# Kernel tuning notes

Hardware: AMD Instinct MI355X
Metric: run time of the kernel (lower is better)

The kernel has to match this reference:

```python
import jax, jax.numpy as jnp
import numpy as np

NUM_HEADS = 4
NUM_LEVELS = 4
NUM_POINTS = 8
EMBED = 256
HEAD_DIM = EMBED // NUM_HEADS
SHAPES = np.array([[92, 160], [46, 80], [23, 40], [12, 20]], dtype=np.int64)  # (h, w) per level
NUM_VALUE = int((SHAPES[:, 0] * SHAPES[:, 1]).sum())  # 19560
DEPTH = 64
NQ = 20000
BS = 1
NZ = 4  # num_Z_anchors; NUM_POINTS % NZ == 0


def _depth_bias():
    # replicates init_smpl_off_weights for sampling_offsets_depth.bias
    th = np.arange(NUM_HEADS) * (2.0 * np.pi / NUM_HEADS)
    g = ((np.cos(th) + np.sin(th)) / 2.0)[:, None, None] * np.ones((NUM_HEADS, NUM_LEVELS, NUM_POINTS))
    g = g * (np.arange(NUM_POINTS) + 1)[None, None, :]
    return jnp.asarray(g.reshape(-1), dtype=jnp.float32)


def setup_inputs() -> dict:
    key = jax.random.key(0)
    ks = jax.random.split(key, 8)
    f = jnp.float32
    s = 0.02
    query = jax.random.normal(ks[0], (BS, NQ, EMBED), f)
    value = jax.random.normal(ks[1], (BS, NUM_VALUE, EMBED), f)
    value_dpt_dist = jax.nn.softmax(jax.random.normal(ks[2], (BS, NUM_VALUE, DEPTH), f), axis=-1)
    reference_points = jax.random.uniform(ks[3], (BS, NQ, NZ, 3), f)
    spatial_shapes = jnp.asarray(SHAPES)
    level_start_index = jnp.asarray(np.concatenate([[0], np.cumsum(SHAPES[:, 0] * SHAPES[:, 1])[:-1]]))
    Wv = jax.random.normal(ks[4], (EMBED, EMBED), f) * s
    bv = jnp.zeros((EMBED,), f)
    Wo = jax.random.normal(ks[5], (EMBED, NUM_HEADS * NUM_LEVELS * NUM_POINTS * 2), f) * s
    bo = jax.random.normal(ks[6], (NUM_HEADS * NUM_LEVELS * NUM_POINTS * 2,), f) * 0.5
    Wod = jnp.zeros((EMBED, NUM_HEADS * NUM_LEVELS * NUM_POINTS), f)  # constant_init 0.0
    bod = _depth_bias()
    Wa = jax.random.normal(ks[7], (EMBED, NUM_HEADS * NUM_LEVELS * NUM_POINTS), f) * s
    ba = jnp.zeros((NUM_HEADS * NUM_LEVELS * NUM_POINTS,), f)
    return dict(query=query, value=value, value_dpt_dist=value_dpt_dist,
                reference_points=reference_points, spatial_shapes=spatial_shapes,
                level_start_index=level_start_index, Wv=Wv, bv=bv, Wo=Wo, bo=bo,
                Wod=Wod, bod=bod, Wa=Wa, ba=ba)


def _forward(query, value, value_dpt_dist, reference_points, spatial_shapes,
             level_start_index, Wv, bv, Wo, bo, Wod, bod, Wa, ba):
    bs, nq, _ = query.shape
    H, L, P = NUM_HEADS, NUM_LEVELS, NUM_POINTS
    dh = HEAD_DIM
    D = value_dpt_dist.shape[-1]
    dt = query.dtype
    shapes = np.asarray(spatial_shapes)  # static level shapes

    v = (value @ Wv + bv).reshape(bs, -1, H, dh)  # value_proj
    off_uv = (query @ Wo + bo).reshape(bs, nq, H, L, P, 2)
    off_d = (query @ Wod + bod).reshape(bs, nq, H, L, P, 1)
    off = jnp.concatenate([off_uv, off_d], axis=-1)  # (bs,nq,H,L,P,3)
    attn = jax.nn.softmax((query @ Wa + ba).reshape(bs, nq, H, L * P), axis=-1)
    attn = attn.reshape(bs, nq, H, L, P)

    # offset_normalizer = (w, h, D) per level
    norm = jnp.asarray(np.stack([shapes[:, 1], shapes[:, 0], np.full(L, D)], -1), dtype=dt)
    off = off / norm[None, None, None, :, None, :]
    Z = reference_points.shape[2]
    off = off.reshape(bs, nq, H, L, P // Z, Z, 3)
    loc = (reference_points[:, :, None, None, None, :, :] + off).reshape(bs, nq, H, L, P, 3)

    starts = np.concatenate([[0], np.cumsum(shapes[:, 0] * shapes[:, 1])]).astype(int)
    gather_bh = jax.vmap(jax.vmap(lambda a, i: a[i]))   # over (bs, heads)
    gather_b = jax.vmap(lambda a, i: a[i])              # over bs

    out = jnp.zeros((bs, nq, H, dh), dt)
    for l in range(L):
        Hl, Wl = int(shapes[l, 0]), int(shapes[l, 1])
        v_l = v[:, starts[l]:starts[l + 1]].transpose(0, 2, 1, 3)          # (bs,H,HW,dh)
        d_l = value_dpt_dist[:, starts[l]:starts[l + 1]].reshape(bs, Hl * Wl * D)
        ll = loc[:, :, :, l]                                               # (bs,nq,H,P,3)
        # grid_sample (align_corners=False) pixel coordinates
        x = ll[..., 0] * Wl - 0.5
        y = ll[..., 1] * Hl - 0.5
        z = ll[..., 2] * D - 0.5
        x0f, y0f, z0f = jnp.floor(x), jnp.floor(y), jnp.floor(z)
        fx, fy, fz = x - x0f, y - y0f, z - z0f
        x0 = x0f.astype(jnp.int32); y0 = y0f.astype(jnp.int32); z0 = z0f.astype(jnp.int32)
        z0c = jnp.clip(z0, 0, D - 1)
        z1c = jnp.clip(z0 + 1, 0, D - 1)
        wz0 = (1.0 - fz) * ((z0 >= 0) & (z0 <= D - 1)).astype(dt)
        wz1 = fz * ((z0 + 1 >= 0) & (z0 + 1 <= D - 1)).astype(dt)

        acc = jnp.zeros((bs, nq, H, P, dh), dt)
        for xi, wx in ((x0, 1.0 - fx), (x0 + 1, fx)):
            for yi, wy in ((y0, 1.0 - fy), (y0 + 1, fy)):
                valid = ((xi >= 0) & (xi < Wl) & (yi >= 0) & (yi < Hl)).astype(dt)
                w_uv = wx * wy * valid                                     # (bs,nq,H,P)
                idx = jnp.clip(yi, 0, Hl - 1) * Wl + jnp.clip(xi, 0, Wl - 1)
                idx_h = idx.transpose(0, 2, 1, 3).reshape(bs, H, nq * P)
                val = gather_bh(v_l, idx_h).reshape(bs, H, nq, P, dh).transpose(0, 2, 1, 3, 4)
                d0 = gather_b(d_l, (idx * D + z0c).reshape(bs, -1)).reshape(bs, nq, H, P)
                d1 = gather_b(d_l, (idx * D + z1c).reshape(bs, -1)).reshape(bs, nq, H, P)
                dscore = wz0 * d0 + wz1 * d1                               # depth lerp at this spatial corner
                acc = acc + (w_uv * dscore)[..., None] * val
        out = out + jnp.einsum('bqhp,bqhpd->bqhd', attn[:, :, :, l], acc)
    return out.reshape(bs, nq, H * dh)


def reference(query, value, value_dpt_dist, reference_points, spatial_shapes,
              level_start_index, Wv, bv, Wo, bo, Wod, bod, Wa, ba):
    return _forward(query, value, value_dpt_dist, reference_points, spatial_shapes,
                    level_start_index, Wv, bv, Wo, bo, Wod, bod, Wa, ba)
```

## Files before the change

### kernel.cpp

```cpp
#include <hip/hip_runtime.h>
#include <math.h>

#define NQ    20000
#define NV    19560
#define NHEAD 4
#define DEPTHD 64

typedef __attribute__((ext_vector_type(8))) short short8;
typedef __attribute__((ext_vector_type(4))) float f32x4;

__device__ __forceinline__ ushort f2bf(float f) {
    uint32_t u = __float_as_uint(f);
    uint32_t r = (u + 0x7FFFu + ((u >> 16) & 1u)) >> 16;
    return (ushort)r;
}
__device__ __forceinline__ float bf_lo(uint32_t d) { return __uint_as_float(d << 16); }
__device__ __forceinline__ float bf_hi(uint32_t d) { return __uint_as_float(d & 0xFFFF0000u); }

__global__ __launch_bounds__(256) void prep_weights(
    const float* __restrict__ Wv, const float* __restrict__ Wo,
    const float* __restrict__ Wod, const float* __restrict__ Wa,
    const float* __restrict__ bo, const float* __restrict__ bod,
    const float* __restrict__ ba,
    ushort* __restrict__ WvT, ushort* __restrict__ WqT, float* __restrict__ bq)
{
    const int b = blockIdx.x;
    const int k = threadIdx.x;
    if (b < 256) {
        WvT[b * 256 + k] = f2bf(Wv[k * 256 + b]);
    } else if (b < 768) {
        const int n = b - 256;
        float w;
        if (n < 256)      w = Wo [k * 256 + n];
        else if (n < 384) w = Wod[k * 128 + (n - 256)];
        else              w = Wa [k * 128 + (n - 384)];
        WqT[n * 256 + k] = f2bf(w);
    } else {
        for (int i = k; i < 512; i += 256) {
            float v;
            if (i < 256)      v = bo[i];
            else if (i < 384) v = bod[i - 256];
            else              v = ba[i - 384];
            bq[i] = v;
        }
    }
}

__global__ __launch_bounds__(256) void prep_ddist(
    const float* __restrict__ ddist, uint32_t* __restrict__ ddist2)
{
    const int idx = blockIdx.x * 256 + threadIdx.x;
    if (idx >= NV * 64) return;
    const int z = idx & 63;
    const float lo = ddist[idx];
    const float hi = ddist[idx + ((z < 63) ? 1 : 0)];
    ddist2[idx] = (uint32_t)f2bf(lo) | ((uint32_t)f2bf(hi) << 16);
}

template<bool BF16_OUT>
__global__ __launch_bounds__(256) void gemm_mfma_bf16(
    const float* __restrict__ A, const ushort* __restrict__ BT,
    const float* __restrict__ bias, void* __restrict__ Cout,
    int M, int ldc)
{
    constexpr int K = 256, BK = 32;
    __shared__ ushort Asb[128][40];
    __shared__ ushort Bsb[128][40];

    const int tid  = threadIdx.x;
    const int lane = tid & 63;
    const int wave = tid >> 6;
    const int wm   = wave >> 1;
    const int wn   = wave & 1;
    const int brow = blockIdx.y * 128;
    const int bcol = blockIdx.x * 128;
    const int l15  = lane & 15;
    const int kg   = lane >> 4;

    f32x4 acc[4][4] = {};

    const int rA    = tid >> 1;
    const int partA = tid & 1;

    for (int k0 = 0; k0 < K; k0 += BK) {
        {
            ushort tmp[16];
            if (brow + rA < M) {
                const float* ap = A + (size_t)(brow + rA) * K + k0 + partA * 16;
                #pragma unroll
                for (int i = 0; i < 4; ++i) {
                    float4 v = *reinterpret_cast<const float4*>(ap + i * 4);
                    tmp[i * 4 + 0] = f2bf(v.x);
                    tmp[i * 4 + 1] = f2bf(v.y);
                    tmp[i * 4 + 2] = f2bf(v.z);
                    tmp[i * 4 + 3] = f2bf(v.w);
                }
            } else {
                #pragma unroll
                for (int i = 0; i < 16; ++i) tmp[i] = 0;
            }
            *reinterpret_cast<uint4*>(&Asb[rA][partA * 16 + 0]) = *reinterpret_cast<uint4*>(tmp);
            *reinterpret_cast<uint4*>(&Asb[rA][partA * 16 + 8]) = *reinterpret_cast<uint4*>(tmp + 8);
        }
        #pragma unroll
        for (int i = 0; i < 2; ++i) {
            int f  = tid + i * 256;
            int n  = f >> 2;
            int c8 = (f & 3) * 8;
            uint4 v = *reinterpret_cast<const uint4*>(BT + (size_t)(bcol + n) * K + k0 + c8);
            *reinterpret_cast<uint4*>(&Bsb[n][c8]) = v;
        }
        __syncthreads();

        short8 af[4], bfv[4];
        #pragma unroll
        for (int mf = 0; mf < 4; ++mf)
            af[mf] = *reinterpret_cast<const short8*>(&Asb[wm * 64 + mf * 16 + l15][kg * 8]);
        #pragma unroll
        for (int nf = 0; nf < 4; ++nf)
            bfv[nf] = *reinterpret_cast<const short8*>(&Bsb[wn * 64 + nf * 16 + l15][kg * 8]);
        #pragma unroll
        for (int mf = 0; mf < 4; ++mf)
            #pragma unroll
            for (int nf = 0; nf < 4; ++nf)
                acc[mf][nf] = __builtin_amdgcn_mfma_f32_16x16x32_bf16(af[mf], bfv[nf], acc[mf][nf], 0, 0, 0);
        __syncthreads();
    }

    #pragma unroll
    for (int mf = 0; mf < 4; ++mf) {
        #pragma unroll
        for (int reg = 0; reg < 4; ++reg) {
            int row = brow + wm * 64 + mf * 16 + kg * 4 + reg;
            if (row >= M) continue;
            #pragma unroll
            for (int nf = 0; nf < 4; ++nf) {
                int col = bcol + wn * 64 + nf * 16 + l15;
                float v = acc[mf][nf][reg] + bias[col];
                if (BF16_OUT)
                    ((ushort*)Cout)[(size_t)row * ldc + col] = f2bf(v);
                else
                    ((float*)Cout)[(size_t)row * ldc + col] = v;
            }
        }
    }
}

__device__ __forceinline__ void fma8(float* acc, float w, uint4 r) {
    acc[0] = fmaf(w, bf_lo(r.x), acc[0]);
    acc[1] = fmaf(w, bf_hi(r.x), acc[1]);
    acc[2] = fmaf(w, bf_lo(r.y), acc[2]);
    acc[3] = fmaf(w, bf_hi(r.y), acc[3]);
    acc[4] = fmaf(w, bf_lo(r.z), acc[4]);
    acc[5] = fmaf(w, bf_hi(r.z), acc[5]);
    acc[6] = fmaf(w, bf_lo(r.w), acc[6]);
    acc[7] = fmaf(w, bf_hi(r.w), acc[7]);
}

__global__ __launch_bounds__(256) void deform_sample(
    const float* __restrict__ qproj,
    const ushort* __restrict__ vproj,
    const uint32_t* __restrict__ ddist2,
    const float* __restrict__ refpts,
    float* __restrict__ out)
{
    const int b    = blockIdx.x;
    const int h    = threadIdx.x >> 6;
    const int lane = threadIdx.x & 63;
    const int j    = lane & 31;
    const int qq   = lane >> 5;
    const int q    = 2 * b + qq;

    __shared__ float2 sm[NHEAD][2][128];

    const float* qrow = qproj + (size_t)q * 512;

    float logit = __builtin_nontemporal_load(qrow + 384 + h * 32 + j);
    float m = logit;
    #pragma unroll
    for (int o = 16; o; o >>= 1) m = fmaxf(m, __shfl_xor(m, o));
    float e = __expf(logit - m);
    float s = e;
    #pragma unroll
    for (int o = 16; o; o >>= 1) s += __shfl_xor(s, o);
    const float aw = e / s;

    const int l  = j >> 3;
    const int p  = j & 7;
    const int zi = p & 3;
    const int Wl = 160 >> l;
    const int Hl = (l == 0) ? 92 : (l == 1) ? 46 : (l == 2) ? 23 : 12;
    const int st = (l == 0) ? 0  : (l == 1) ? 14720 : (l == 2) ? 18400 : 19320;

    const int oidx = (h * 4 + l) * 8 + p;
    const float ox = __builtin_nontemporal_load(qrow + oidx * 2 + 0);
    const float oy = __builtin_nontemporal_load(qrow + oidx * 2 + 1);
    const float od = __builtin_nontemporal_load(qrow + 256 + oidx);
    const float rx = refpts[(q * 4 + zi) * 3 + 0];
    const float ry = refpts[(q * 4 + zi) * 3 + 1];
    const float rz = refpts[(q * 4 + zi) * 3 + 2];

    const float x = fmaf(rx, (float)Wl, ox - 0.5f);
    const float y = fmaf(ry, (float)Hl, oy - 0.5f);
    const float z = fmaf(rz, 64.0f,     od - 0.5f);
    const float x0f = floorf(x), y0f = floorf(y), z0f = floorf(z);
    const float fx = x - x0f, fy = y - y0f, fz = z - z0f;
    const int x0 = (int)x0f, y0 = (int)y0f, z0 = (int)z0f;

    const int z0c = min(max(z0, 0), DEPTHD - 1);
    const float wlo = (z0 >= 0 && z0 <= 63) ? (1.f - fz) : ((z0 == -1) ? fz : 0.f);
    const float whi = (z0 >= 0 && z0 <= 62) ? fz : 0.f;

    #pragma unroll
    for (int c = 0; c < 4; ++c) {
        const int   cy = c >> 1, cx = c & 1;
        const int   yi = y0 + cy, xi = x0 + cx;
        const float wy = cy ? fy : (1.f - fy);
        const float wx = cx ? fx : (1.f - fx);
        const bool  valid = (xi >= 0) & (xi < Wl) & (yi >= 0) & (yi < Hl);
        const int   yc = min(max(yi, 0), Hl - 1);
        const int   xc = min(max(xi, 0), Wl - 1);
        const int   row = st + yc * Wl + xc;
        const uint32_t pd = ddist2[row * 64 + z0c];
        const float dscore = wlo * bf_lo(pd) + whi * bf_hi(pd);
        const float coef = valid ? (aw * wx * wy * dscore) : 0.f;
        sm[h][qq][c * 32 + j] = make_float2(coef, __int_as_float(row * 512 + h * 128));
    }

    const int g   = lane >> 3;
    const int ch8 = (lane & 7) << 3;
    const uint32_t chb = (uint32_t)(ch8 << 1);
    const char* vb = (const char*)vproj;
    const float2* s0 = sm[h][0];
    const float2* s1 = sm[h][1];

    float acc0[8] = {}, acc1[8] = {};
    uint4 rA[8], rB[8];

    #pragma unroll
    for (int t = 0; t < 8; ++t) {
        const float2 w = s0[t * 8 + g];
        rA[t] = *reinterpret_cast<const uint4*>(vb + ((uint32_t)__float_as_int(w.y) + chb));
    }
    #pragma unroll
    for (int t = 0; t < 8; ++t) {
        const float2 w = s1[t * 8 + g];
        rB[t] = *reinterpret_cast<const uint4*>(vb + ((uint32_t)__float_as_int(w.y) + chb));
    }
    #pragma unroll
    for (int t = 0; t < 8; ++t) {
        fma8(acc0, s0[t * 8 + g].x, rA[t]);
        const float2 w = s0[(t + 8) * 8 + g];
        rA[t] = *reinterpret_cast<const uint4*>(vb + ((uint32_t)__float_as_int(w.y) + chb));
    }
    #pragma unroll
    for (int t = 0; t < 8; ++t) {
        fma8(acc1, s1[t * 8 + g].x, rB[t]);
        const float2 w = s1[(t + 8) * 8 + g];
        rB[t] = *reinterpret_cast<const uint4*>(vb + ((uint32_t)__float_as_int(w.y) + chb));
    }
    #pragma unroll
    for (int t = 0; t < 8; ++t) fma8(acc0, s0[(t + 8) * 8 + g].x, rA[t]);
    #pragma unroll
    for (int t = 0; t < 8; ++t) fma8(acc1, s1[(t + 8) * 8 + g].x, rB[t]);

    #pragma unroll
    for (int o = 8; o <= 32; o <<= 1) {
        #pragma unroll
        for (int k = 0; k < 8; ++k) {
            acc0[k] += __shfl_xor(acc0[k], o);
            acc1[k] += __shfl_xor(acc1[k], o);
        }
    }

    if (g == 0) {
        float* op0 = out + (size_t)(2 * b) * 256 + h * 64 + ch8;
        f32x4 o00 = {acc0[0], acc0[1], acc0[2], acc0[3]};
        f32x4 o01 = {acc0[4], acc0[5], acc0[6], acc0[7]};
        __builtin_nontemporal_store(o00, reinterpret_cast<f32x4*>(op0));
        __builtin_nontemporal_store(o01, reinterpret_cast<f32x4*>(op0 + 4));
        float* op1 = op0 + 256;
        f32x4 o10 = {acc1[0], acc1[1], acc1[2], acc1[3]};
        f32x4 o11 = {acc1[4], acc1[5], acc1[6], acc1[7]};
        __builtin_nontemporal_store(o10, reinterpret_cast<f32x4*>(op1));
        __builtin_nontemporal_store(o11, reinterpret_cast<f32x4*>(op1 + 4));
    }
}

extern "C" void kernel_launch(void* const* d_in, const int* in_sizes, int n_in,
                              void* d_out, int out_size, void* d_ws, size_t ws_size,
                              hipStream_t stream)
{
    const float* query  = (const float*)d_in[0];
    const float* value  = (const float*)d_in[1];
    const float* ddist  = (const float*)d_in[2];
    const float* refpts = (const float*)d_in[3];
    const float* Wv  = (const float*)d_in[6];
    const float* bv  = (const float*)d_in[7];
    const float* Wo  = (const float*)d_in[8];
    const float* bo  = (const float*)d_in[9];
    const float* Wod = (const float*)d_in[10];
    const float* bod = (const float*)d_in[11];
    const float* Wa  = (const float*)d_in[12];
    const float* ba  = (const float*)d_in[13];
    float* out = (float*)d_out;

    char* ws = (char*)d_ws;
    ushort*   vbuf   = (ushort*)ws;
    float*    qbuf   = (float*)(ws + 10014720);
    ushort*   WvT    = (ushort*)(ws + 10014720 + 40960000);
    ushort*   WqT    = WvT + 256 * 256;
    float*    bq     = (float*)(WqT + 512 * 256);
    uint32_t* ddist2 = (uint32_t*)((char*)bq + 2048);

    dim3 blk(256);

    prep_weights<<<dim3(769), blk, 0, stream>>>(Wv, Wo, Wod, Wa, bo, bod, ba, WvT, WqT, bq);
    prep_ddist<<<dim3((NV * 64 + 255) / 256), blk, 0, stream>>>(ddist, ddist2);

    gemm_mfma_bf16<true><<<dim3(2, (NV + 127) / 128), blk, 0, stream>>>(
        value, WvT, bv, vbuf, NV, 256);

    gemm_mfma_bf16<false><<<dim3(4, (NQ + 127) / 128), blk, 0, stream>>>(
        query, WqT, bq, qbuf, NQ, 512);

    deform_sample<<<dim3(NQ / 2), blk, 0, stream>>>(qbuf, vbuf, ddist2, refpts, out);
}
```

Measured before the change: 155.2 us.

## Repack depth distribution into z-major plane with paired x-neighbors for fewer gathers

The depth-distribution prep now transposes to a z-major layout where each entry packs the bf16 pair (z, z+1) for two horizontally adjacent pixels. The sampler then fetches two 8-byte loads per point instead of four scattered 4-byte gathers, and selects the x0/x1 corner from each pair. The softmax is moved after these loads are issued so its latency overlaps them, and sched_barriers plus a launch-bounds occupancy hint constrain scheduling. The prep kernel becomes a shared-memory transpose, which costs extra work, and the larger workspace entries (uint2) double the buffer footprint.

```diff
diff --git a/kernel.cpp b/kernel.cpp
--- a/kernel.cpp
+++ b/kernel.cpp
@@ -46,15 +46,28 @@
     }
 }
 
-__global__ __launch_bounds__(256) void prep_ddist(
-    const float* __restrict__ ddist, uint32_t* __restrict__ ddist2)
-{
-    const int idx = blockIdx.x * 256 + threadIdx.x;
-    if (idx >= NV * 64) return;
-    const int z = idx & 63;
-    const float lo = ddist[idx];
-    const float hi = ddist[idx + ((z < 63) ? 1 : 0)];
-    ddist2[idx] = (uint32_t)f2bf(lo) | ((uint32_t)f2bf(hi) << 16);
+__global__ __launch_bounds__(256) void prep_dd4(
+    const float* __restrict__ dd, uint2* __restrict__ dd4)
+{
+    __shared__ float tile[33][65];
+    const int r0 = blockIdx.x * 32;
+    for (int i = threadIdx.x; i < 33 * 64; i += 256) {
+        const int rr = i >> 6, zz = i & 63;
+        const int gr = min(r0 + rr, NV - 1);
+        tile[rr][zz] = dd[(size_t)gr * 64 + zz];
+    }
+    __syncthreads();
+    for (int i = threadIdx.x; i < 32 * 64; i += 256) {
+        const int zz = i >> 5;
+        const int rr = i & 31;
+        if (r0 + rr < NV) {
+            const int z1 = min(zz + 1, 63);
+            uint2 o;
+            o.x = (uint32_t)f2bf(tile[rr][zz])     | ((uint32_t)f2bf(tile[rr][z1])     << 16);
+            o.y = (uint32_t)f2bf(tile[rr + 1][zz]) | ((uint32_t)f2bf(tile[rr + 1][z1]) << 16);
+            dd4[(size_t)zz * NV + r0 + rr] = o;
+        }
+    }
 }
 
 template<bool BF16_OUT>
@@ -157,10 +170,10 @@
     acc[7] = fmaf(w, bf_hi(r.w), acc[7]);
 }
 
-__global__ __launch_bounds__(256) void deform_sample(
+__global__ __launch_bounds__(256, 4) void deform_sample(
     const float* __restrict__ qproj,
     const ushort* __restrict__ vproj,
-    const uint32_t* __restrict__ ddist2,
+    const uint2* __restrict__ dd4,
     const float* __restrict__ refpts,
     float* __restrict__ out)
 {
@@ -174,16 +187,6 @@
     __shared__ float2 sm[NHEAD][2][128];
 
     const float* qrow = qproj + (size_t)q * 512;
-
-    float logit = __builtin_nontemporal_load(qrow + 384 + h * 32 + j);
-    float m = logit;
-    #pragma unroll
-    for (int o = 16; o; o >>= 1) m = fmaxf(m, __shfl_xor(m, o));
-    float e = __expf(logit - m);
-    float s = e;
-    #pragma unroll
-    for (int o = 16; o; o >>= 1) s += __shfl_xor(s, o);
-    const float aw = e / s;
 
     const int l  = j >> 3;
     const int p  = j & 7;
@@ -211,20 +214,58 @@
     const float wlo = (z0 >= 0 && z0 <= 63) ? (1.f - fz) : ((z0 == -1) ? fz : 0.f);
     const float whi = (z0 >= 0 && z0 <= 62) ? fz : 0.f;
 
-    #pragma unroll
-    for (int c = 0; c < 4; ++c) {
-        const int   cy = c >> 1, cx = c & 1;
-        const int   yi = y0 + cy, xi = x0 + cx;
-        const float wy = cy ? fy : (1.f - fy);
-        const float wx = cx ? fx : (1.f - fx);
-        const bool  valid = (xi >= 0) & (xi < Wl) & (yi >= 0) & (yi < Hl);
-        const int   yc = min(max(yi, 0), Hl - 1);
-        const int   xc = min(max(xi, 0), Wl - 1);
-        const int   row = st + yc * Wl + xc;
-        const uint32_t pd = ddist2[row * 64 + z0c];
-        const float dscore = wlo * bf_lo(pd) + whi * bf_hi(pd);
-        const float coef = valid ? (aw * wx * wy * dscore) : 0.f;
-        sm[h][qq][c * 32 + j] = make_float2(coef, __int_as_float(row * 512 + h * 128));
+    const int yc0 = min(max(y0, 0), Hl - 1);
+    const int yc1 = min(max(y0 + 1, 0), Hl - 1);
+    const int xb  = min(max(x0, 0), Wl - 2);
+    const int xc0 = min(max(x0, 0), Wl - 1);
+    const int xc1 = min(max(x0 + 1, 0), Wl - 1);
+    const int s0i = xc0 - xb;
+    const int s1i = xc1 - xb;
+
+    const uint2* plane = dd4 + (size_t)z0c * NV + st + xb;
+    const uint2 u0 = plane[yc0 * Wl];
+    const uint2 u1 = plane[yc1 * Wl];
+
+    float logit = __builtin_nontemporal_load(qrow + 384 + h * 32 + j);
+    float m = logit;
+    #pragma unroll
+    for (int o = 16; o; o >>= 1) m = fmaxf(m, __shfl_xor(m, o));
+    float e = __expf(logit - m);
+    float s = e;
+    #pragma unroll
+    for (int o = 16; o; o >>= 1) s += __shfl_xor(s, o);
+    const float aw = e / s;
+
+    const float wx0 = 1.f - fx, wx1 = fx;
+    const float wy0 = 1.f - fy, wy1 = fy;
+    const bool vx0 = (x0 >= 0) & (x0 < Wl);
+    const bool vx1 = (x0 + 1 >= 0) & (x0 + 1 < Wl);
+    const bool vy0 = (y0 >= 0) & (y0 < Hl);
+    const bool vy1 = (y0 + 1 >= 0) & (y0 + 1 < Hl);
+
+    const uint32_t pd00 = s0i ? u0.y : u0.x;
+    const uint32_t pd01 = s1i ? u0.y : u0.x;
+    const uint32_t pd10 = s0i ? u1.y : u1.x;
+    const uint32_t pd11 = s1i ? u1.y : u1.x;
+
+    const int r00 = st + yc0 * Wl + xc0;
+    const int r01 = st + yc0 * Wl + xc1;
+    const int r10 = st + yc1 * Wl + xc0;
+    const int r11 = st + yc1 * Wl + xc1;
+
+    {
+        const float ds00 = wlo * bf_lo(pd00) + whi * bf_hi(pd00);
+        const float ds01 = wlo * bf_lo(pd01) + whi * bf_hi(pd01);
+        const float ds10 = wlo * bf_lo(pd10) + whi * bf_hi(pd10);
+        const float ds11 = wlo * bf_lo(pd11) + whi * bf_hi(pd11);
+        const float c00 = (vx0 && vy0) ? (aw * wx0 * wy0 * ds00) : 0.f;
+        const float c01 = (vx1 && vy0) ? (aw * wx1 * wy0 * ds01) : 0.f;
+        const float c10 = (vx0 && vy1) ? (aw * wx0 * wy1 * ds10) : 0.f;
+        const float c11 = (vx1 && vy1) ? (aw * wx1 * wy1 * ds11) : 0.f;
+        sm[h][qq][0 * 32 + j] = make_float2(c00, __int_as_float(r00 * 512 + h * 128));
+        sm[h][qq][1 * 32 + j] = make_float2(c01, __int_as_float(r01 * 512 + h * 128));
+        sm[h][qq][2 * 32 + j] = make_float2(c10, __int_as_float(r10 * 512 + h * 128));
+        sm[h][qq][3 * 32 + j] = make_float2(c11, __int_as_float(r11 * 512 + h * 128));
     }
 
     const int g   = lane >> 3;
@@ -238,27 +279,27 @@
     uint4 rA[8], rB[8];
 
     #pragma unroll
-    for (int t = 0; t < 8; ++t) {
-        const float2 w = s0[t * 8 + g];
-        rA[t] = *reinterpret_cast<const uint4*>(vb + ((uint32_t)__float_as_int(w.y) + chb));
-    }
-    #pragma unroll
-    for (int t = 0; t < 8; ++t) {
-        const float2 w = s1[t * 8 + g];
-        rB[t] = *reinterpret_cast<const uint4*>(vb + ((uint32_t)__float_as_int(w.y) + chb));
-    }
+    for (int t = 0; t < 8; ++t)
+        rA[t] = *reinterpret_cast<const uint4*>(vb + ((uint32_t)__float_as_int(s0[t * 8 + g].y) + chb));
+    #pragma unroll
+    for (int t = 0; t < 8; ++t)
+        rB[t] = *reinterpret_cast<const uint4*>(vb + ((uint32_t)__float_as_int(s1[t * 8 + g].y) + chb));
+    __builtin_amdgcn_sched_barrier(0);
+
     #pragma unroll
     for (int t = 0; t < 8; ++t) {
         fma8(acc0, s0[t * 8 + g].x, rA[t]);
-        const float2 w = s0[(t + 8) * 8 + g];
-        rA[t] = *reinterpret_cast<const uint4*>(vb + ((uint32_t)__float_as_int(w.y) + chb));
-    }
+        rA[t] = *reinterpret_cast<const uint4*>(vb + ((uint32_t)__float_as_int(s0[(t + 8) * 8 + g].y) + chb));
+    }
+    __builtin_amdgcn_sched_barrier(0);
+
     #pragma unroll
     for (int t = 0; t < 8; ++t) {
         fma8(acc1, s1[t * 8 + g].x, rB[t]);
-        const float2 w = s1[(t + 8) * 8 + g];
-        rB[t] = *reinterpret_cast<const uint4*>(vb + ((uint32_t)__float_as_int(w.y) + chb));
-    }
+        rB[t] = *reinterpret_cast<const uint4*>(vb + ((uint32_t)__float_as_int(s1[(t + 8) * 8 + g].y) + chb));
+    }
+    __builtin_amdgcn_sched_barrier(0);
+
     #pragma unroll
     for (int t = 0; t < 8; ++t) fma8(acc0, s0[(t + 8) * 8 + g].x, rA[t]);
     #pragma unroll
@@ -306,17 +347,17 @@
     float* out = (float*)d_out;
 
     char* ws = (char*)d_ws;
-    ushort*   vbuf   = (ushort*)ws;
-    float*    qbuf   = (float*)(ws + 10014720);
-    ushort*   WvT    = (ushort*)(ws + 10014720 + 40960000);
-    ushort*   WqT    = WvT + 256 * 256;
-    float*    bq     = (float*)(WqT + 512 * 256);
-    uint32_t* ddist2 = (uint32_t*)((char*)bq + 2048);
+    ushort* vbuf = (ushort*)ws;
+    float*  qbuf = (float*)(ws + 10014720);
+    ushort* WvT  = (ushort*)(ws + 10014720 + 40960000);
+    ushort* WqT  = WvT + 256 * 256;
+    float*  bq   = (float*)(WqT + 512 * 256);
+    uint2*  dd4  = (uint2*)((char*)bq + 2048);
 
     dim3 blk(256);
 
     prep_weights<<<dim3(769), blk, 0, stream>>>(Wv, Wo, Wod, Wa, bo, bod, ba, WvT, WqT, bq);
-    prep_ddist<<<dim3((NV * 64 + 255) / 256), blk, 0, stream>>>(ddist, ddist2);
+    prep_dd4<<<dim3((NV + 31) / 32), blk, 0, stream>>>(ddist, dd4);
 
     gemm_mfma_bf16<true><<<dim3(2, (NV + 127) / 128), blk, 0, stream>>>(
         value, WvT, bv, vbuf, NV, 256);
@@ -324,5 +365,5 @@
     gemm_mfma_bf16<false><<<dim3(4, (NQ + 127) / 128), blk, 0, stream>>>(
         query, WqT, bq, qbuf, NQ, 512);
 
-    deform_sample<<<dim3(NQ / 2), blk, 0, stream>>>(qbuf, vbuf, ddist2, refpts, out);
-}
+    deform_sample<<<dim3(NQ / 2), blk, 0, stream>>>(qbuf, vbuf, dd4, refpts, out);
+}
```

Measured after the change: 294.3 us. 1.9x slower.
